# Optimization experiments

Hardware: AMD Instinct MI355X
Metric: run time of the kernel (lower is better)

Reference implementation:

```python
import jax, jax.numpy as jnp
import numpy as np

B, S, D = 16, 1024, 1024
E = 8            # num routed experts
I_MOE = 2048     # moe_intermediate_size
I_SH = 2048      # shared_expert_intermediate_size
TOP_K = 2
K_CAP = max(1, min(int(S / E * TOP_K), S))  # tokens kept per expert = 256
UNCOND_LABEL = 1000
INIT_STD = 0.02


def _l2norm(x, axis=-1, eps=1e-12):
    # matches F.normalize(p=2): x / max(||x||, eps)
    n = jnp.sqrt(jnp.sum(x * x, axis=axis, keepdims=True))
    return x / jnp.maximum(n, eps)


def _mlp(x, Wg, Wu, Wd):
    # gated SiLU MLP: down(silu(gate(x)) * up(x))
    return (jax.nn.silu(x @ Wg) * (x @ Wu)) @ Wd


def setup_inputs() -> dict:
    key = jax.random.key(0)
    ks = jax.random.split(key, 12)
    hidden_states = jax.random.normal(ks[0], (B, S, D), dtype=jnp.float32)
    labels = jax.random.randint(ks[1], (B,), 0, 1001, dtype=jnp.int64)
    cluster_centers = jax.random.normal(ks[2], (E, D), dtype=jnp.float32) * INIT_STD
    sc = 0.02
    # routed experts stacked along E
    Wg = jax.random.normal(ks[3], (E, D, I_MOE), dtype=jnp.float32) * sc
    Wu = jax.random.normal(ks[4], (E, D, I_MOE), dtype=jnp.float32) * sc
    Wd = jax.random.normal(ks[5], (E, I_MOE, D), dtype=jnp.float32) * sc
    # uncond expert (experts[-1])
    u_Wg = jax.random.normal(ks[6], (D, I_MOE), dtype=jnp.float32) * sc
    u_Wu = jax.random.normal(ks[7], (D, I_MOE), dtype=jnp.float32) * sc
    u_Wd = jax.random.normal(ks[8], (I_MOE, D), dtype=jnp.float32) * sc
    # shared expert
    s_Wg = jax.random.normal(ks[9], (D, I_SH), dtype=jnp.float32) * sc
    s_Wu = jax.random.normal(ks[10], (D, I_SH), dtype=jnp.float32) * sc
    s_Wd = jax.random.normal(ks[11], (I_SH, D), dtype=jnp.float32) * sc
    return dict(hidden_states=hidden_states, labels=labels,
                cluster_centers=cluster_centers, Wg=Wg, Wu=Wu, Wd=Wd,
                u_Wg=u_Wg, u_Wu=u_Wu, u_Wd=u_Wd,
                s_Wg=s_Wg, s_Wu=s_Wu, s_Wd=s_Wd)


def reference(hidden_states, labels, cluster_centers, Wg, Wu, Wd,
              u_Wg, u_Wu, u_Wd, s_Wg, s_Wu, s_Wd):
    Bc, Sc, Dc = hidden_states.shape
    # ---- router: cosine similarity, softmax over tokens, expert-choice top-k ----
    x_n = _l2norm(hidden_states)                 # (B,S,D)
    c_n = _l2norm(cluster_centers)               # (E,D)
    cos_sim = jnp.einsum('bsd,ed->bes', x_n, c_n)  # expert view (B,E,S)
    cond_weights = jax.nn.softmax(cos_sim, axis=-1)  # softmax over S
    gating, idx = jax.lax.top_k(cond_weights, K_CAP)  # (B,E,k) each; sums, so sort order irrelevant
    # ---- dispatch (gather replaces one-hot einsum) ----
    expert_inputs = jnp.take_along_axis(hidden_states[:, None, :, :],
                                        idx[..., None], axis=2)   # (B,E,k,D)
    # ---- per-expert gated MLP as grouped GEMM ----
    h = jax.nn.silu(jnp.einsum('bekd,edi->beki', expert_inputs, Wg)) * \
        jnp.einsum('bekd,edi->beki', expert_inputs, Wu)
    expert_outputs = jnp.einsum('beki,eid->bekd', h, Wd)          # (B,E,k,D)
    # ---- weighted combine (scatter-add replaces one-hot einsum) ----
    weighted = gating[..., None] * expert_outputs                  # (B,E,k,D)
    cond_output = jnp.zeros_like(hidden_states).at[
        jnp.arange(Bc)[:, None], idx.reshape(Bc, -1)
    ].add(weighted.reshape(Bc, -1, Dc))                            # (B,S,D)
    # ---- uncond expert path, selected per batch by label ----
    uncond_output = _mlp(hidden_states, u_Wg, u_Wu, u_Wd)
    cond_mask = (labels != UNCOND_LABEL)[:, None, None]
    final_output = jnp.where(cond_mask, cond_output, uncond_output)
    # ---- shared expert ----
    final_output = final_output + _mlp(hidden_states, s_Wg, s_Wu, s_Wd)
    return final_output
```

## Files before the change

### kernel.cpp

```cpp
#include <hip/hip_runtime.h>
#include <stdint.h>

typedef __bf16 bf16;
typedef __attribute__((ext_vector_type(8))) __bf16 bf16x8;
typedef __attribute__((ext_vector_type(4))) float f32x4;

__device__ __forceinline__ void async_copy16(void* lds, const void* gp) {
    __builtin_amdgcn_global_load_lds(
        (__attribute__((address_space(1))) void*)(gp),
        (__attribute__((address_space(3))) void*)(lds), 16, 0, 0);
}

__device__ __forceinline__ const bf16* lread(const bf16* base, int R, int lq) {
    return base + R * 32 + (((lq + (R >> 1)) & 3) << 3);
}

__device__ __forceinline__ void xcd_remap(int& bx, int& by, int& bz) {
    int gx = gridDim.x, gy = gridDim.y, gz = gridDim.z;
    int panels = gy * gz;
    if (panels & 7) { bx = blockIdx.x; by = blockIdx.y; bz = blockIdx.z; return; }
    int L = (blockIdx.z * gy + blockIdx.y) * gx + blockIdx.x;
    int X = L & 7, S = L >> 3;
    bx = S % gx;
    int P = S / gx;
    int byT = X * (panels >> 3) + P;
    bz = byT / gy;
    by = byT % gy;
}


__global__ __launch_bounds__(256) void cnorm_kernel(const float* __restrict__ centers,
                                                    float* __restrict__ invc) {
    int e = blockIdx.x, t = threadIdx.x;
    float4 v = ((const float4*)(centers + (size_t)e * 1024))[t];
    float ss = v.x * v.x + v.y * v.y + v.z * v.z + v.w * v.w;
    #pragma unroll
    for (int o = 32; o; o >>= 1) ss += __shfl_down(ss, o);
    __shared__ float red[4];
    if ((t & 63) == 0) red[t >> 6] = ss;
    __syncthreads();
    if (t == 0) invc[e] = 1.f / fmaxf(sqrtf(red[0] + red[1] + red[2] + red[3]), 1e-12f);
}

__global__ __launch_bounds__(256) void router_convert_kernel(
    const float* __restrict__ X, const float* __restrict__ centers,
    const float* __restrict__ invc, bf16* __restrict__ hid, float* __restrict__ P) {
    int tok = blockIdx.x, t = threadIdx.x;
    int b = tok >> 10, s = tok & 1023;
    float4 v = ((const float4*)(X + (size_t)tok * 1024))[t];
    union { bf16 h[4]; uint2 u; } cv;
    cv.h[0] = (bf16)v.x; cv.h[1] = (bf16)v.y; cv.h[2] = (bf16)v.z; cv.h[3] = (bf16)v.w;
    ((uint2*)(hid + (size_t)tok * 1024))[t] = cv.u;
    float ss = v.x * v.x + v.y * v.y + v.z * v.z + v.w * v.w;
    float dots[8];
    #pragma unroll
    for (int e = 0; e < 8; e++) {
        float4 c = ((const float4*)(centers + (size_t)e * 1024))[t];
        dots[e] = v.x * c.x + v.y * c.y + v.z * c.z + v.w * c.w;
    }
    #pragma unroll
    for (int o = 32; o; o >>= 1) {
        ss += __shfl_down(ss, o);
        #pragma unroll
        for (int e = 0; e < 8; e++) dots[e] += __shfl_down(dots[e], o);
    }
    __shared__ float red[4][9];
    if ((t & 63) == 0) {
        red[t >> 6][0] = ss;
        #pragma unroll
        for (int e = 0; e < 8; e++) red[t >> 6][1 + e] = dots[e];
    }
    __syncthreads();
    if (t < 8) {
        float S = red[0][0] + red[1][0] + red[2][0] + red[3][0];
        float rinv = 1.f / fmaxf(sqrtf(S), 1e-12f);
        float d = red[0][1 + t] + red[1][1 + t] + red[2][1 + t] + red[3][1 + t];
        P[((size_t)(b * 8 + t) << 10) + s] = d * rinv * invc[t];
    }
}

__global__ __launch_bounds__(256) void softmax_kernel(float* __restrict__ P) {
    int row = blockIdx.x, t = threadIdx.x;
    float4* p4 = (float4*)(P + ((size_t)row << 10));
    float4 v = p4[t];
    float mx = fmaxf(fmaxf(v.x, v.y), fmaxf(v.z, v.w));
    #pragma unroll
    for (int o = 32; o; o >>= 1) mx = fmaxf(mx, __shfl_down(mx, o));
    __shared__ float red[8];
    if ((t & 63) == 0) red[t >> 6] = mx;
    __syncthreads();
    float M = fmaxf(fmaxf(red[0], red[1]), fmaxf(red[2], red[3]));
    float e0 = expf(v.x - M), e1 = expf(v.y - M), e2 = expf(v.z - M), e3 = expf(v.w - M);
    float s = e0 + e1 + e2 + e3;
    #pragma unroll
    for (int o = 32; o; o >>= 1) s += __shfl_down(s, o);
    if ((t & 63) == 0) red[4 + (t >> 6)] = s;
    __syncthreads();
    float inv = 1.f / (red[4] + red[5] + red[6] + red[7]);
    p4[t] = make_float4(e0 * inv, e1 * inv, e2 * inv, e3 * inv);
}

__global__ __launch_bounds__(256) void zero_cnt_kernel(int* __restrict__ cnt) {
    cnt[blockIdx.x * 256 + threadIdx.x] = 0;
}

__global__ __launch_bounds__(1024) void topk_kernel(const float* __restrict__ P,
                                                    int* __restrict__ row_map,
                                                    float* __restrict__ gsc,
                                                    int* __restrict__ cnt,
                                                    int* __restrict__ inv) {
    int row = blockIdx.x, t = threadIdx.x;
    __shared__ unsigned long long keys[1024];
    float v = P[((size_t)row << 10) + t];
    unsigned u = __float_as_uint(v);
    u = (u & 0x80000000u) ? ~u : (u | 0x80000000u);
    keys[t] = ((unsigned long long)u << 32) | (unsigned)(~t);
    __syncthreads();
    for (int k = 2; k <= 1024; k <<= 1) {
        for (int j = k >> 1; j > 0; j >>= 1) {
            int ixj = t ^ j;
            if (ixj > t) {
                bool up = ((t & k) == 0);
                unsigned long long a = keys[t], b = keys[ixj];
                if ((a > b) == up) { keys[t] = b; keys[ixj] = a; }
            }
            __syncthreads();
        }
    }
    if (t >= 768) {
        int slot = t - 768;
        int s = (int)(~(unsigned)keys[t]) & 1023;
        int b = row >> 3, e = row & 7;
        int m = e * 4096 + b * 256 + slot;
        int tok = b * 1024 + s;
        row_map[m] = tok;
        gsc[m] = P[((size_t)row << 10) + s];
        int pos = atomicAdd(cnt + tok, 1);
        inv[tok * 8 + pos] = m;
    }
}


__global__ __launch_bounds__(256) void transpose_cvt(
    const float* __restrict__ srcA, bf16* __restrict__ dstA, int batchA,
    const float* __restrict__ srcB, bf16* __restrict__ dstB, int R, int C) {
    int z = blockIdx.z;
    const float* src; bf16* dst;
    if (z < batchA) { src = srcA + (size_t)z * R * C; dst = dstA + (size_t)z * R * C; }
    else            { src = srcB + (size_t)(z - batchA) * R * C; dst = dstB + (size_t)(z - batchA) * R * C; }
    __shared__ float tile[32][33];
    int tx = threadIdx.x & 31, ty = threadIdx.x >> 5;
    int c0 = blockIdx.x * 32, r0 = blockIdx.y * 32;
    #pragma unroll
    for (int p = 0; p < 4; p++) {
        int r = p * 8 + ty;
        tile[r][tx] = src[(size_t)(r0 + r) * C + c0 + tx];
    }
    __syncthreads();
    #pragma unroll
    for (int p = 0; p < 4; p++) {
        int cl = p * 8 + ty;
        dst[(size_t)(c0 + cl) * R + r0 + tx] = (bf16)tile[tx][cl];
    }
}


__global__ __launch_bounds__(256) void gateup_kernel(
    const bf16* __restrict__ X, const int* __restrict__ row_map,
    const bf16* __restrict__ WgT, const bf16* __restrict__ WuT,
    bf16* __restrict__ H, int Mz, int m_base, const int* __restrict__ labels, int mode) {
    int bx, by, z; xcd_remap(bx, by, z);
    if (mode == 1) { int b = (m_base + by * 128) >> 10; if (labels[b] != 1000) return; }
    if (mode == 2) { int b = (m_base + by * 128) >> 8;  if (labels[b] == 1000) return; }
    __shared__ bf16 lds[8192];
    bf16* As = lds; bf16* Bg = lds + 4096; bf16* Bu = lds + 6144;
    const int t = threadIdx.x;
    const bf16* Wg_e = WgT + (size_t)z * 2048 * 1024;
    const bf16* Wu_e = WuT + (size_t)z * 2048 * 1024;
    bf16* H_e = H + (size_t)z * Mz * 2048;

    const int m0 = by * 128, n0 = bx * 64;
    const int r = t >> 2;
    const int ce = (((t & 3) - (t >> 3)) & 3) * 8;
    int tok0, tok1;
    if (mode == 2) {
        const int* rm = row_map + (size_t)z * Mz;
        tok0 = rm[m0 + r]; tok1 = rm[m0 + 64 + r];
    } else { tok0 = m_base + m0 + r; tok1 = m_base + m0 + 64 + r; }
    const bf16* pa0 = X + (size_t)tok0 * 1024 + ce;
    const bf16* pa1 = X + (size_t)tok1 * 1024 + ce;
    const bf16* pg  = Wg_e + (size_t)(n0 + r) * 1024 + ce;
    const bf16* pu  = Wu_e + (size_t)(n0 + r) * 1024 + ce;
    bf16* lA0 = As + t * 8; bf16* lA1 = As + 2048 + t * 8;
    bf16* lBg = Bg + t * 8; bf16* lBu = Bu + t * 8;

    const int l = t & 63, w = t >> 6;
    const int wm = w >> 1, wn = w & 1;
    const int lr = l & 15, lq = l >> 4;

    f32x4 accg[4][2] = {}, accu[4][2] = {};
    for (int kt = 0; kt < 1024; kt += 32) {
        __syncthreads();
        async_copy16(lA0, pa0); async_copy16(lA1, pa1);
        async_copy16(lBg, pg);  async_copy16(lBu, pu);
        pa0 += 32; pa1 += 32; pg += 32; pu += 32;
        __syncthreads();
        bf16x8 a[4], bg[2], bu[2];
        #pragma unroll
        for (int mi = 0; mi < 4; mi++)
            a[mi] = *(const bf16x8*)lread(As, wm * 64 + mi * 16 + lr, lq);
        #pragma unroll
        for (int ni = 0; ni < 2; ni++) {
            bg[ni] = *(const bf16x8*)lread(Bg, wn * 32 + ni * 16 + lr, lq);
            bu[ni] = *(const bf16x8*)lread(Bu, wn * 32 + ni * 16 + lr, lq);
        }
        #pragma unroll
        for (int mi = 0; mi < 4; mi++)
            #pragma unroll
            for (int ni = 0; ni < 2; ni++) {
                accg[mi][ni] = __builtin_amdgcn_mfma_f32_16x16x32_bf16(a[mi], bg[ni], accg[mi][ni], 0, 0, 0);
                accu[mi][ni] = __builtin_amdgcn_mfma_f32_16x16x32_bf16(a[mi], bu[ni], accu[mi][ni], 0, 0, 0);
            }
    }
    #pragma unroll
    for (int mi = 0; mi < 4; mi++)
        #pragma unroll
        for (int ni = 0; ni < 2; ni++)
            #pragma unroll
            for (int rr = 0; rr < 4; rr++) {
                int m = m0 + wm * 64 + mi * 16 + lq * 4 + rr;
                int n = n0 + wn * 32 + ni * 16 + lr;
                float g = accg[mi][ni][rr], uu = accu[mi][ni][rr];
                float h = g / (1.f + __expf(-g)) * uu;
                H_e[(size_t)m * 2048 + n] = (bf16)h;
            }
}


__global__ __launch_bounds__(256) void down_kernel(
    const bf16* __restrict__ Hbase, const bf16* __restrict__ WdT,
    float* __restrict__ out, bf16* __restrict__ stage, int Mz, int m_base,
    const int* __restrict__ row_map, const float* __restrict__ gsc,
    const int* __restrict__ labels, int mode) {
    int bx, by, z; xcd_remap(bx, by, z);
    if (mode == 1) { int b = (m_base + by * 128) >> 10; if (labels[b] != 1000) return; }
    if (mode >= 2) { int b = (m_base + by * 128) >> 8;  if (labels[b] == 1000) return; }
    __shared__ bf16 lds[8192];
    bf16* As = lds; bf16* Bs = lds + 4096;
    const int t = threadIdx.x;
    const bf16* A_e = Hbase + (size_t)z * Mz * 2048;
    const bf16* B_e = WdT + (size_t)z * 1024 * 2048;
    const int m0 = by * 128, n0 = bx * 128;
    const int r = t >> 2;
    const int ce = (((t & 3) - (t >> 3)) & 3) * 8;
    const bf16* pa0 = A_e + (size_t)(m0 + r) * 2048 + ce;
    const bf16* pa1 = A_e + (size_t)(m0 + 64 + r) * 2048 + ce;
    const bf16* pb0 = B_e + (size_t)(n0 + r) * 2048 + ce;
    const bf16* pb1 = B_e + (size_t)(n0 + 64 + r) * 2048 + ce;
    bf16* lA0 = As + t * 8; bf16* lA1 = As + 2048 + t * 8;
    bf16* lB0 = Bs + t * 8; bf16* lB1 = Bs + 2048 + t * 8;

    const int l = t & 63, w = t >> 6;
    const int wm = w >> 1, wn = w & 1;
    const int lr = l & 15, lq = l >> 4;

    f32x4 acc[4][4] = {};
    for (int kt = 0; kt < 2048; kt += 32) {
        __syncthreads();
        async_copy16(lA0, pa0); async_copy16(lA1, pa1);
        async_copy16(lB0, pb0); async_copy16(lB1, pb1);
        pa0 += 32; pa1 += 32; pb0 += 32; pb1 += 32;
        __syncthreads();
        bf16x8 a[4], bb[4];
        #pragma unroll
        for (int mi = 0; mi < 4; mi++)
            a[mi] = *(const bf16x8*)lread(As, wm * 64 + mi * 16 + lr, lq);
        #pragma unroll
        for (int ni = 0; ni < 4; ni++)
            bb[ni] = *(const bf16x8*)lread(Bs, wn * 64 + ni * 16 + lr, lq);
        #pragma unroll
        for (int mi = 0; mi < 4; mi++)
            #pragma unroll
            for (int ni = 0; ni < 4; ni++)
                acc[mi][ni] = __builtin_amdgcn_mfma_f32_16x16x32_bf16(a[mi], bb[ni], acc[mi][ni], 0, 0, 0);
    }
    float gs[4][4];
    if (mode >= 2) {
        #pragma unroll
        for (int mi = 0; mi < 4; mi++)
            #pragma unroll
            for (int rr = 0; rr < 4; rr++)
                gs[mi][rr] = gsc[(size_t)z * Mz + m0 + wm * 64 + mi * 16 + lq * 4 + rr];
    }
    #pragma unroll
    for (int mi = 0; mi < 4; mi++)
        #pragma unroll
        for (int ni = 0; ni < 4; ni++)
            #pragma unroll
            for (int rr = 0; rr < 4; rr++) {
                int m = m0 + wm * 64 + mi * 16 + lq * 4 + rr;
                int n = n0 + wn * 64 + ni * 16 + lr;
                float v = acc[mi][ni][rr];
                if (mode == 0) {
                    out[(size_t)(m_base + m) * 1024 + n] = v;
                } else if (mode == 1) {
                    out[(size_t)(m_base + m) * 1024 + n] += v;
                } else if (mode == 2) {
                    size_t em = (size_t)z * Mz + m;
                    stage[em * 1024 + n] = (bf16)(v * gs[mi][rr]);
                } else {
                    size_t em = (size_t)z * Mz + m;
                    int tok = row_map[em];
                    atomicAdd(out + (size_t)tok * 1024 + n, v * gs[mi][rr]);
                }
            }
}


__global__ __launch_bounds__(256) void combine_kernel(
    const bf16* __restrict__ stage, const int* __restrict__ cnt,
    const int* __restrict__ inv, const int* __restrict__ labels,
    float* __restrict__ out) {
    int tok = blockIdx.x;
    if (labels[tok >> 10] == 1000) return;
    int c = cnt[tok];
    if (c == 0) return;
    int t = threadIdx.x;
    float4* o4 = (float4*)(out + (size_t)tok * 1024);
    float4 acc = o4[t];
    for (int i = 0; i < c; i++) {
        int m = inv[tok * 8 + i];
        ushort4 raw = *(const ushort4*)(stage + (size_t)m * 1024 + t * 4);
        acc.x += __uint_as_float((unsigned)raw.x << 16);
        acc.y += __uint_as_float((unsigned)raw.y << 16);
        acc.z += __uint_as_float((unsigned)raw.z << 16);
        acc.w += __uint_as_float((unsigned)raw.w << 16);
    }
    o4[t] = acc;
}


extern "C" void kernel_launch(void* const* d_in, const int* in_sizes, int n_in,
                              void* d_out, int out_size, void* d_ws, size_t ws_size,
                              hipStream_t stream) {
    (void)in_sizes; (void)n_in; (void)out_size;
    const float* X       = (const float*)d_in[0];
    const int*   labels  = (const int*)d_in[1];
    const float* centers = (const float*)d_in[2];
    const float* Wg  = (const float*)d_in[3];
    const float* Wu  = (const float*)d_in[4];
    const float* Wd  = (const float*)d_in[5];
    const float* uWg = (const float*)d_in[6];
    const float* uWu = (const float*)d_in[7];
    const float* uWd = (const float*)d_in[8];
    const float* sWg = (const float*)d_in[9];
    const float* sWu = (const float*)d_in[10];
    const float* sWd = (const float*)d_in[11];
    float* out = (float*)d_out;

    char* w = (char*)d_ws;
    auto alloc = [&](size_t n) { char* p = w; w += (n + 255) & ~(size_t)255; return p; };
    bf16* hid  = (bf16*)alloc((size_t)16384 * 1024 * 2);
    bf16* WgT  = (bf16*)alloc((size_t)8 * 2048 * 1024 * 2);
    bf16* WuT  = (bf16*)alloc((size_t)8 * 2048 * 1024 * 2);
    bf16* WdT  = (bf16*)alloc((size_t)8 * 2048 * 1024 * 2);
    bf16* uWgT = (bf16*)alloc((size_t)2048 * 1024 * 2);
    bf16* uWuT = (bf16*)alloc((size_t)2048 * 1024 * 2);
    bf16* uWdT = (bf16*)alloc((size_t)2048 * 1024 * 2);
    bf16* sWgT = (bf16*)alloc((size_t)2048 * 1024 * 2);
    bf16* sWuT = (bf16*)alloc((size_t)2048 * 1024 * 2);
    bf16* sWdT = (bf16*)alloc((size_t)2048 * 1024 * 2);
    float* P     = (float*)alloc((size_t)128 * 1024 * 4);
    float* invc  = (float*)alloc(256);
    int*   rmap  = (int*)alloc((size_t)32768 * 4);
    float* gsc   = (float*)alloc((size_t)32768 * 4);
    int*   cnt   = (int*)alloc((size_t)16384 * 4);
    int*   inv   = (int*)alloc((size_t)16384 * 8 * 4);

    size_t used0 = (size_t)(w - (char*)d_ws);
    size_t rem0  = ws_size > used0 ? ws_size - used0 : 0;
    const size_t STAGE_BYTES = (size_t)32768 * 1024 * 2;
    const size_t HMIN_BYTES  = (size_t)8192 * 2048 * 2;
    bf16* stage = nullptr;
    if (rem0 >= STAGE_BYTES + HMIN_BYTES)
        stage = (bf16*)alloc(STAGE_BYTES);

    size_t used = (size_t)(w - (char*)d_ws);
    size_t hcap = ws_size > used ? ws_size - used : 0;
    bf16* H = (bf16*)w;
    long maxRows = (long)(hcap / ((size_t)2048 * 2));
    int CR = (int)(maxRows < 16384 ? maxRows : 16384);
    CR &= ~127;
    if (CR < 128) CR = 128;
    int EPG = 0;
    if (maxRows >= 32768) EPG = 8;
    else if (maxRows >= 16384) EPG = 4;
    else if (maxRows >= 8192)  EPG = 2;
    else if (maxRows >= 4096)  EPG = 1;

    const size_t WSTRIDE = (size_t)2048 * 1024;
    const int rmode = stage ? 2 : 3;

    cnorm_kernel<<<8, 256, 0, stream>>>(centers, invc);
    router_convert_kernel<<<16384, 256, 0, stream>>>(X, centers, invc, hid, P);
    softmax_kernel<<<128, 256, 0, stream>>>(P);
    zero_cnt_kernel<<<64, 256, 0, stream>>>(cnt);
    topk_kernel<<<128, 1024, 0, stream>>>(P, rmap, gsc, cnt, inv);
    transpose_cvt<<<dim3(64, 32, 16), 256, 0, stream>>>(Wg, WgT, 8, Wu, WuT, 1024, 2048);
    transpose_cvt<<<dim3(32, 64, 8), 256, 0, stream>>>(Wd, WdT, 8, nullptr, nullptr, 2048, 1024);
    transpose_cvt<<<dim3(64, 32, 2), 256, 0, stream>>>(uWg, uWgT, 1, sWg, sWgT, 1024, 2048);
    transpose_cvt<<<dim3(64, 32, 2), 256, 0, stream>>>(uWu, uWuT, 1, sWu, sWuT, 1024, 2048);
    transpose_cvt<<<dim3(32, 64, 2), 256, 0, stream>>>(uWd, uWdT, 1, sWd, sWdT, 2048, 1024);

    for (int m0 = 0; m0 < 16384; m0 += CR) {
        int rows = (16384 - m0 < CR) ? 16384 - m0 : CR;
        gateup_kernel<<<dim3(32, rows / 128, 1), 256, 0, stream>>>(
            hid, nullptr, sWgT, sWuT, H, rows, m0, labels, 0);
        down_kernel<<<dim3(8, rows / 128, 1), 256, 0, stream>>>(
            H, sWdT, out, nullptr, rows, m0, nullptr, nullptr, labels, 0);
    }
    for (int m0 = 0; m0 < 16384; m0 += CR) {
        int rows = (16384 - m0 < CR) ? 16384 - m0 : CR;
        gateup_kernel<<<dim3(32, rows / 128, 1), 256, 0, stream>>>(
            hid, nullptr, uWgT, uWuT, H, rows, m0, labels, 1);
        down_kernel<<<dim3(8, rows / 128, 1), 256, 0, stream>>>(
            H, uWdT, out, nullptr, rows, m0, nullptr, nullptr, labels, 1);
    }
    if (EPG > 0) {
        for (int g = 0; g < 8; g += EPG) {
            gateup_kernel<<<dim3(32, 32, EPG), 256, 0, stream>>>(
                hid, rmap + (size_t)g * 4096, WgT + (size_t)g * WSTRIDE,
                WuT + (size_t)g * WSTRIDE, H, 4096, 0, labels, 2);
            down_kernel<<<dim3(8, 32, EPG), 256, 0, stream>>>(
                H, WdT + (size_t)g * WSTRIDE, out,
                stage ? stage + (size_t)g * 4096 * 1024 : nullptr, 4096, 0,
                rmap + (size_t)g * 4096, gsc + (size_t)g * 4096, labels, rmode);
        }
    } else {
        for (int e = 0; e < 8; e++) {
            for (int m0 = 0; m0 < 4096; m0 += CR) {
                int rows = (4096 - m0 < CR) ? 4096 - m0 : CR;
                gateup_kernel<<<dim3(32, rows / 128, 1), 256, 0, stream>>>(
                    hid, rmap + (size_t)e * 4096 + m0, WgT + (size_t)e * WSTRIDE,
                    WuT + (size_t)e * WSTRIDE, H, rows, m0, labels, 2);
                down_kernel<<<dim3(8, rows / 128, 1), 256, 0, stream>>>(
                    H, WdT + (size_t)e * WSTRIDE, out,
                    stage ? stage + ((size_t)e * 4096 + m0) * 1024 : nullptr, rows, m0,
                    rmap + (size_t)e * 4096 + m0, gsc + (size_t)e * 4096 + m0, labels, rmode);
            }
        }
    }
    if (stage)
        combine_kernel<<<16384, 256, 0, stream>>>(stage, cnt, inv, labels, out);
}
```

Measured before the change: 1.247 ms.

## Double-buffer LDS and enlarge GEMM tiles to 256 rows with 512 threads

The gate/up and down GEMM kernels now run 512-thread blocks that cover 256x128 and 256x256 output tiles, twice as many rows and columns per block as before. The single LDS buffer with two barriers per k-step becomes a double-buffered pipeline: the async loads for the next k-slice are issued before the MFMAs on the current one, with one barrier per step. The larger tiles are meant to raise arithmetic intensity, and the double buffering is meant to hide global-to-LDS latency. In exchange, 64 KB of LDS and larger accumulator arrays per block lower occupancy, and the grid shrinks to a handful of blocks per chunk, which risks underfilling the GPU.

After: 1.098 ms. -12.0%, faster.

```diff
diff --git a/kernel.cpp b/kernel.cpp
--- a/kernel.cpp
+++ b/kernel.cpp
@@ -165,70 +165,83 @@
 }
 
 
-__global__ __launch_bounds__(256) void gateup_kernel(
+
+__global__ __launch_bounds__(512) void gateup_kernel(
     const bf16* __restrict__ X, const int* __restrict__ row_map,
     const bf16* __restrict__ WgT, const bf16* __restrict__ WuT,
     bf16* __restrict__ H, int Mz, int m_base, const int* __restrict__ labels, int mode) {
     int bx, by, z; xcd_remap(bx, by, z);
-    if (mode == 1) { int b = (m_base + by * 128) >> 10; if (labels[b] != 1000) return; }
-    if (mode == 2) { int b = (m_base + by * 128) >> 8;  if (labels[b] == 1000) return; }
-    __shared__ bf16 lds[8192];
-    bf16* As = lds; bf16* Bg = lds + 4096; bf16* Bu = lds + 6144;
+    if (mode == 1) { int b = (m_base + by * 256) >> 10; if (labels[b] != 1000) return; }
+    if (mode == 2) { int b = (m_base + by * 256) >> 8;  if (labels[b] == 1000) return; }
+    __shared__ bf16 lds[2 * 16384];
     const int t = threadIdx.x;
     const bf16* Wg_e = WgT + (size_t)z * 2048 * 1024;
     const bf16* Wu_e = WuT + (size_t)z * 2048 * 1024;
     bf16* H_e = H + (size_t)z * Mz * 2048;
 
-    const int m0 = by * 128, n0 = bx * 64;
+    const int m0 = by * 256, n0 = bx * 128;
     const int r = t >> 2;
     const int ce = (((t & 3) - (t >> 3)) & 3) * 8;
     int tok0, tok1;
     if (mode == 2) {
         const int* rm = row_map + (size_t)z * Mz;
-        tok0 = rm[m0 + r]; tok1 = rm[m0 + 64 + r];
-    } else { tok0 = m_base + m0 + r; tok1 = m_base + m0 + 64 + r; }
+        tok0 = rm[m0 + r]; tok1 = rm[m0 + 128 + r];
+    } else { tok0 = m_base + m0 + r; tok1 = m_base + m0 + 128 + r; }
     const bf16* pa0 = X + (size_t)tok0 * 1024 + ce;
     const bf16* pa1 = X + (size_t)tok1 * 1024 + ce;
     const bf16* pg  = Wg_e + (size_t)(n0 + r) * 1024 + ce;
     const bf16* pu  = Wu_e + (size_t)(n0 + r) * 1024 + ce;
-    bf16* lA0 = As + t * 8; bf16* lA1 = As + 2048 + t * 8;
-    bf16* lBg = Bg + t * 8; bf16* lBu = Bu + t * 8;
 
     const int l = t & 63, w = t >> 6;
-    const int wm = w >> 1, wn = w & 1;
+    const int wm = w >> 2, wn = w & 3;
     const int lr = l & 15, lq = l >> 4;
 
-    f32x4 accg[4][2] = {}, accu[4][2] = {};
-    for (int kt = 0; kt < 1024; kt += 32) {
-        __syncthreads();
-        async_copy16(lA0, pa0); async_copy16(lA1, pa1);
-        async_copy16(lBg, pg);  async_copy16(lBu, pu);
+    f32x4 accg[8][2] = {}, accu[8][2] = {};
+
+    auto STAGE = [&](int s) {
+        bf16* L = lds + s * 16384;
+        async_copy16(L + t * 8, pa0);
+        async_copy16(L + 4096 + t * 8, pa1);
+        async_copy16(L + 8192 + t * 8, pg);
+        async_copy16(L + 12288 + t * 8, pu);
         pa0 += 32; pa1 += 32; pg += 32; pu += 32;
-        __syncthreads();
-        bf16x8 a[4], bg[2], bu[2];
-        #pragma unroll
-        for (int mi = 0; mi < 4; mi++)
-            a[mi] = *(const bf16x8*)lread(As, wm * 64 + mi * 16 + lr, lq);
+    };
+
+    const int NT = 1024 / 32;
+    STAGE(0);
+    __syncthreads();
+    int cur = 0;
+    for (int kt = 0; kt < NT; ++kt) {
+        if (kt + 1 < NT) STAGE(cur ^ 1);
+        const bf16* As = lds + cur * 16384;
+        const bf16* Bg = As + 8192;
+        const bf16* Bu = As + 12288;
+        bf16x8 a[8], bg[2], bu[2];
+        #pragma unroll
+        for (int mi = 0; mi < 8; mi++)
+            a[mi] = *(const bf16x8*)lread(As, wm * 128 + mi * 16 + lr, lq);
         #pragma unroll
         for (int ni = 0; ni < 2; ni++) {
             bg[ni] = *(const bf16x8*)lread(Bg, wn * 32 + ni * 16 + lr, lq);
             bu[ni] = *(const bf16x8*)lread(Bu, wn * 32 + ni * 16 + lr, lq);
         }
         #pragma unroll
-        for (int mi = 0; mi < 4; mi++)
+        for (int mi = 0; mi < 8; mi++)
             #pragma unroll
             for (int ni = 0; ni < 2; ni++) {
                 accg[mi][ni] = __builtin_amdgcn_mfma_f32_16x16x32_bf16(a[mi], bg[ni], accg[mi][ni], 0, 0, 0);
                 accu[mi][ni] = __builtin_amdgcn_mfma_f32_16x16x32_bf16(a[mi], bu[ni], accu[mi][ni], 0, 0, 0);
             }
-    }
-    #pragma unroll
-    for (int mi = 0; mi < 4; mi++)
+        __syncthreads();
+        cur ^= 1;
+    }
+    #pragma unroll
+    for (int mi = 0; mi < 8; mi++)
         #pragma unroll
         for (int ni = 0; ni < 2; ni++)
             #pragma unroll
             for (int rr = 0; rr < 4; rr++) {
-                int m = m0 + wm * 64 + mi * 16 + lq * 4 + rr;
+                int m = m0 + wm * 128 + mi * 16 + lq * 4 + rr;
                 int n = n0 + wn * 32 + ni * 16 + lr;
                 float g = accg[mi][ni][rr], uu = accu[mi][ni][rr];
                 float h = g / (1.f + __expf(-g)) * uu;
@@ -237,68 +250,79 @@
 }
 
 
-__global__ __launch_bounds__(256) void down_kernel(
+__global__ __launch_bounds__(512) void down_kernel(
     const bf16* __restrict__ Hbase, const bf16* __restrict__ WdT,
     float* __restrict__ out, bf16* __restrict__ stage, int Mz, int m_base,
     const int* __restrict__ row_map, const float* __restrict__ gsc,
     const int* __restrict__ labels, int mode) {
     int bx, by, z; xcd_remap(bx, by, z);
-    if (mode == 1) { int b = (m_base + by * 128) >> 10; if (labels[b] != 1000) return; }
-    if (mode >= 2) { int b = (m_base + by * 128) >> 8;  if (labels[b] == 1000) return; }
-    __shared__ bf16 lds[8192];
-    bf16* As = lds; bf16* Bs = lds + 4096;
+    if (mode == 1) { int b = (m_base + by * 256) >> 10; if (labels[b] != 1000) return; }
+    if (mode >= 2) { int b = (m_base + by * 256) >> 8;  if (labels[b] == 1000) return; }
+    __shared__ bf16 lds[2 * 16384];
     const int t = threadIdx.x;
     const bf16* A_e = Hbase + (size_t)z * Mz * 2048;
     const bf16* B_e = WdT + (size_t)z * 1024 * 2048;
-    const int m0 = by * 128, n0 = bx * 128;
+    const int m0 = by * 256, n0 = bx * 256;
     const int r = t >> 2;
     const int ce = (((t & 3) - (t >> 3)) & 3) * 8;
     const bf16* pa0 = A_e + (size_t)(m0 + r) * 2048 + ce;
-    const bf16* pa1 = A_e + (size_t)(m0 + 64 + r) * 2048 + ce;
+    const bf16* pa1 = A_e + (size_t)(m0 + 128 + r) * 2048 + ce;
     const bf16* pb0 = B_e + (size_t)(n0 + r) * 2048 + ce;
-    const bf16* pb1 = B_e + (size_t)(n0 + 64 + r) * 2048 + ce;
-    bf16* lA0 = As + t * 8; bf16* lA1 = As + 2048 + t * 8;
-    bf16* lB0 = Bs + t * 8; bf16* lB1 = Bs + 2048 + t * 8;
+    const bf16* pb1 = B_e + (size_t)(n0 + 128 + r) * 2048 + ce;
 
     const int l = t & 63, w = t >> 6;
-    const int wm = w >> 1, wn = w & 1;
+    const int wm = w >> 2, wn = w & 3;
     const int lr = l & 15, lq = l >> 4;
 
-    f32x4 acc[4][4] = {};
-    for (int kt = 0; kt < 2048; kt += 32) {
-        __syncthreads();
-        async_copy16(lA0, pa0); async_copy16(lA1, pa1);
-        async_copy16(lB0, pb0); async_copy16(lB1, pb1);
+    f32x4 acc[8][4] = {};
+
+    auto STAGE = [&](int s) {
+        bf16* L = lds + s * 16384;
+        async_copy16(L + t * 8, pa0);
+        async_copy16(L + 4096 + t * 8, pa1);
+        async_copy16(L + 8192 + t * 8, pb0);
+        async_copy16(L + 12288 + t * 8, pb1);
         pa0 += 32; pa1 += 32; pb0 += 32; pb1 += 32;
-        __syncthreads();
-        bf16x8 a[4], bb[4];
-        #pragma unroll
-        for (int mi = 0; mi < 4; mi++)
-            a[mi] = *(const bf16x8*)lread(As, wm * 64 + mi * 16 + lr, lq);
+    };
+
+    const int NT = 2048 / 32;
+    STAGE(0);
+    __syncthreads();
+    int cur = 0;
+    for (int kt = 0; kt < NT; ++kt) {
+        if (kt + 1 < NT) STAGE(cur ^ 1);
+        const bf16* As = lds + cur * 16384;
+        const bf16* Bs = As + 8192;
+        bf16x8 a[8], bb[4];
+        #pragma unroll
+        for (int mi = 0; mi < 8; mi++)
+            a[mi] = *(const bf16x8*)lread(As, wm * 128 + mi * 16 + lr, lq);
         #pragma unroll
         for (int ni = 0; ni < 4; ni++)
             bb[ni] = *(const bf16x8*)lread(Bs, wn * 64 + ni * 16 + lr, lq);
         #pragma unroll
-        for (int mi = 0; mi < 4; mi++)
+        for (int mi = 0; mi < 8; mi++)
             #pragma unroll
             for (int ni = 0; ni < 4; ni++)
                 acc[mi][ni] = __builtin_amdgcn_mfma_f32_16x16x32_bf16(a[mi], bb[ni], acc[mi][ni], 0, 0, 0);
-    }
-    float gs[4][4];
+        __syncthreads();
+        cur ^= 1;
+    }
+    float gs[8][4];
     if (mode >= 2) {
         #pragma unroll
-        for (int mi = 0; mi < 4; mi++)
+        for (int mi = 0; mi < 8; mi++)
             #pragma unroll
             for (int rr = 0; rr < 4; rr++)
-                gs[mi][rr] = gsc[(size_t)z * Mz + m0 + wm * 64 + mi * 16 + lq * 4 + rr];
-    }
-    #pragma unroll
-    for (int mi = 0; mi < 4; mi++)
+                gs[mi][rr] = gsc[(size_t)z * Mz + m0 + wm * 128 + mi * 16 + lq * 4 + rr];
+    }
+    #pragma unroll
+    for (int mi = 0; mi < 8; mi++)
         #pragma unroll
         for (int ni = 0; ni < 4; ni++)
             #pragma unroll
             for (int rr = 0; rr < 4; rr++) {
-                int m = m0 + wm * 64 + mi * 16 + lq * 4 + rr;
+                int m = m0 + wm * 128 + mi * 16 + lq * 4 + rr;
                 int n = n0 + wn * 64 + ni * 16 + lr;
                 float v = acc[mi][ni][rr];
                 if (mode == 0) {
@@ -390,8 +414,8 @@
     bf16* H = (bf16*)w;
     long maxRows = (long)(hcap / ((size_t)2048 * 2));
     int CR = (int)(maxRows < 16384 ? maxRows : 16384);
-    CR &= ~127;
-    if (CR < 128) CR = 128;
+    CR &= ~255;
+    if (CR < 256) CR = 256;
     int EPG = 0;
     if (maxRows >= 32768) EPG = 8;
     else if (maxRows >= 16384) EPG = 4;
@@ -414,24 +438,24 @@
 
     for (int m0 = 0; m0 < 16384; m0 += CR) {
         int rows = (16384 - m0 < CR) ? 16384 - m0 : CR;
-        gateup_kernel<<<dim3(32, rows / 128, 1), 256, 0, stream>>>(
+        gateup_kernel<<<dim3(16, rows / 256, 1), 512, 0, stream>>>(
             hid, nullptr, sWgT, sWuT, H, rows, m0, labels, 0);
-        down_kernel<<<dim3(8, rows / 128, 1), 256, 0, stream>>>(
+        down_kernel<<<dim3(4, rows / 256, 1), 512, 0, stream>>>(
             H, sWdT, out, nullptr, rows, m0, nullptr, nullptr, labels, 0);
     }
     for (int m0 = 0; m0 < 16384; m0 += CR) {
         int rows = (16384 - m0 < CR) ? 16384 - m0 : CR;
-        gateup_kernel<<<dim3(32, rows / 128, 1), 256, 0, stream>>>(
+        gateup_kernel<<<dim3(16, rows / 256, 1), 512, 0, stream>>>(
             hid, nullptr, uWgT, uWuT, H, rows, m0, labels, 1);
-        down_kernel<<<dim3(8, rows / 128, 1), 256, 0, stream>>>(
+        down_kernel<<<dim3(4, rows / 256, 1), 512, 0, stream>>>(
             H, uWdT, out, nullptr, rows, m0, nullptr, nullptr, labels, 1);
     }
     if (EPG > 0) {
         for (int g = 0; g < 8; g += EPG) {
-            gateup_kernel<<<dim3(32, 32, EPG), 256, 0, stream>>>(
+            gateup_kernel<<<dim3(16, 16, EPG), 512, 0, stream>>>(
                 hid, rmap + (size_t)g * 4096, WgT + (size_t)g * WSTRIDE,
                 WuT + (size_t)g * WSTRIDE, H, 4096, 0, labels, 2);
-            down_kernel<<<dim3(8, 32, EPG), 256, 0, stream>>>(
+            down_kernel<<<dim3(4, 16, EPG), 512, 0, stream>>>(
                 H, WdT + (size_t)g * WSTRIDE, out,
                 stage ? stage + (size_t)g * 4096 * 1024 : nullptr, 4096, 0,
                 rmap + (size_t)g * 4096, gsc + (size_t)g * 4096, labels, rmode);
@@ -440,10 +464,10 @@
         for (int e = 0; e < 8; e++) {
             for (int m0 = 0; m0 < 4096; m0 += CR) {
                 int rows = (4096 - m0 < CR) ? 4096 - m0 : CR;
-                gateup_kernel<<<dim3(32, rows / 128, 1), 256, 0, stream>>>(
+                gateup_kernel<<<dim3(16, rows / 256, 1), 512, 0, stream>>>(
                     hid, rmap + (size_t)e * 4096 + m0, WgT + (size_t)e * WSTRIDE,
                     WuT + (size_t)e * WSTRIDE, H, rows, m0, labels, 2);
-                down_kernel<<<dim3(8, rows / 128, 1), 256, 0, stream>>>(
+                down_kernel<<<dim3(4, rows / 256, 1), 512, 0, stream>>>(
                     H, WdT + (size_t)e * WSTRIDE, out,
                     stage ? stage + ((size_t)e * 4096 + m0) * 1024 : nullptr, rows, m0,
                     rmap + (size_t)e * 4096 + m0, gsc + (size_t)e * 4096 + m0, labels, rmode);
```
